# Performance work log

Measured on AMD Instinct MI355X. Metric: run time of the kernel, lower is better.

## Reference

```python
import jax, jax.numpy as jnp
import numpy as np

NUM_NODES = 20000
HIDDEN = 64
NUM_EDGES = 640000
LEAK = 0.2  # PyG GATConv negative_slope default


def gat_conv(x, w, a_src, a_dst, b, src, dst, n):
    # x: [N, F_in]; w: [F_in, H*C]; a_src/a_dst: [H, C]; edges j=src -> i=dst
    H, C = a_src.shape
    xe = (x @ w).reshape(n, H, C)                         # [N, H, C]
    es = jnp.einsum('nhc,hc->nh', xe, a_src)              # alpha_src per node
    ed = jnp.einsum('nhc,hc->nh', xe, a_dst)              # alpha_dst per node
    e = jax.nn.leaky_relu(es[src] + ed[dst], LEAK)        # [E, H] edge logits
    # segment softmax over each destination's incoming edges
    m = jax.ops.segment_max(e, dst, num_segments=n)
    p = jnp.exp(e - m[dst])
    s = jax.ops.segment_sum(p, dst, num_segments=n)
    alpha = p / s[dst]                                    # [E, H]
    out = jax.ops.segment_sum(alpha[:, :, None] * xe[src], dst, num_segments=n)
    return out.reshape(n, H * C) + b                      # concat heads + bias


def setup_inputs() -> dict:
    key = jax.random.key(0)
    ks = jax.random.split(key, 16)
    B, S, N, Hd = 4, 12, NUM_NODES, HIDDEN
    sc = 0.1
    inp = {}
    inp['x'] = jax.random.normal(ks[0], (B, S, N), jnp.float32)
    inp['edge_index'] = jax.random.randint(ks[1], (2, NUM_EDGES), 0, N, jnp.int32)
    inp['proj_w'] = jax.random.normal(ks[2], (S, Hd), jnp.float32) * sc
    inp['proj_b'] = jnp.zeros((Hd,), jnp.float32)
    inp['gat0_w'] = jax.random.normal(ks[3], (Hd, Hd), jnp.float32) * sc
    inp['gat0_asrc'] = jax.random.normal(ks[4], (8, 8), jnp.float32) * sc
    inp['gat0_adst'] = jax.random.normal(ks[5], (8, 8), jnp.float32) * sc
    inp['gat0_b'] = jnp.zeros((Hd,), jnp.float32)
    inp['gat1_w'] = jax.random.normal(ks[6], (Hd, Hd), jnp.float32) * sc
    inp['gat1_asrc'] = jax.random.normal(ks[7], (8, 8), jnp.float32) * sc
    inp['gat1_adst'] = jax.random.normal(ks[8], (8, 8), jnp.float32) * sc
    inp['gat1_b'] = jnp.zeros((Hd,), jnp.float32)
    inp['gat2_w'] = jax.random.normal(ks[9], (Hd, Hd), jnp.float32) * sc
    inp['gat2_asrc'] = jax.random.normal(ks[10], (1, Hd), jnp.float32) * sc
    inp['gat2_adst'] = jax.random.normal(ks[11], (1, Hd), jnp.float32) * sc
    inp['gat2_b'] = jnp.zeros((Hd,), jnp.float32)
    inp['conv_w'] = jax.random.normal(ks[12], (Hd, Hd, 3), jnp.float32) * sc
    inp['conv_b'] = jnp.zeros((Hd,), jnp.float32)
    inp['out_w'] = jax.random.normal(ks[13], (Hd, 3), jnp.float32) * sc
    inp['out_b'] = jnp.zeros((3,), jnp.float32)
    return inp


def reference(x, edge_index, proj_w, proj_b,
              gat0_w, gat0_asrc, gat0_adst, gat0_b,
              gat1_w, gat1_asrc, gat1_adst, gat1_b,
              gat2_w, gat2_asrc, gat2_adst, gat2_b,
              conv_w, conv_b, out_w, out_b):
    B, S, N = x.shape
    # PyG GATConv add_self_loops=True
    loops = jnp.arange(N, dtype=edge_index.dtype)
    src = jnp.concatenate([edge_index[0], loops])
    dst = jnp.concatenate([edge_index[1], loops])
    h = jnp.transpose(x, (0, 2, 1)) @ proj_w + proj_b     # [B, N, Hd]
    layers = [(gat0_w, gat0_asrc, gat0_adst, gat0_b),
              (gat1_w, gat1_asrc, gat1_adst, gat1_b),
              (gat2_w, gat2_asrc, gat2_adst, gat2_b)]
    for i, (w, asr, ads, b) in enumerate(layers):
        h = jax.vmap(lambda hb: gat_conv(hb, w, asr, ads, b, src, dst, N))(h)
        if i < len(layers) - 1:
            h = jax.nn.elu(h)                             # dropout is identity in eval
    hc = jnp.transpose(h, (0, 2, 1))                      # [B, Hd, N]
    hc = jax.lax.conv_general_dilated(hc, conv_w, (1,), ((1, 1),),
                                      dimension_numbers=('NCH', 'OIH', 'NCH'))
    hc = jax.nn.relu(hc + conv_b[None, :, None])
    h = jnp.transpose(hc, (0, 2, 1)) @ out_w + out_b      # [B, N, pred]
    return jnp.transpose(h, (0, 2, 1))                    # [B, pred, N]
```

## Files before the change

### kernel.cpp

```cpp
#include <hip/hip_runtime.h>
#include <math.h>

constexpr int B  = 4;
constexpr int S  = 12;
constexpr int N  = 20000;
constexpr int HD = 64;
constexpr int E0 = 640000;
constexpr int EL = E0 + N;
constexpr int BN = B * N;
constexpr int CAP = 128;

__global__ void scatter_kernel(const int* __restrict__ ei, int* __restrict__ cnt,
                               int* __restrict__ perm) {
    int e = blockIdx.x * blockDim.x + threadIdx.x;
    if (e >= EL) return;
    int s, d;
    if (e < E0) { s = ei[e]; d = ei[E0 + e]; }
    else        { s = e - E0; d = s; }
    int pos = atomicAdd(&cnt[d], 1) & (CAP - 1);
    perm[d * CAP + pos] = s;
}

__global__ void tw_kernel(const float* __restrict__ cw, float* __restrict__ cwD) {
    int i = blockIdx.x * blockDim.x + threadIdx.x;
    if (i >= HD * HD * 3) return;
    int o = i / (HD * 3), rem = i % (HD * 3), c = rem / 3, dt = rem % 3;
    cwD[dt * (HD * HD) + c * HD + o] = cw[i];
}

constexpr int GT = 64;

template<int H>
__global__ __launch_bounds__(256, 4)
void gemm_attn_kernel(const float* __restrict__ hin, const float* __restrict__ w,
                      const float* __restrict__ asrc, const float* __restrict__ adst,
                      float* __restrict__ xe, float* __restrict__ es, float* __restrict__ ed) {
    __shared__ float tile[GT * HD];
    int base = blockIdx.x * GT;
    for (int i = threadIdx.x; i < GT * (HD / 4); i += 256)
        ((float4*)tile)[i] = ((const float4*)(hin + (size_t)base * HD))[i];
    int lane = threadIdx.x & 63;
    float wres[HD];
    #pragma unroll
    for (int c = 0; c < HD; ++c) wres[c] = w[c * HD + lane];
    float as_ = asrc[lane], ad_ = adst[lane];
    __syncthreads();
    int wvid = threadIdx.x >> 6;
    for (int j = wvid * 16; j < wvid * 16 + 16; ++j) {
        int t = base + j;
        float acc = 0.f;
        #pragma unroll
        for (int cq = 0; cq < 16; ++cq) {
            float4 r = ((const float4*)tile)[j * 16 + cq];
            acc = fmaf(r.x, wres[4 * cq + 0], acc);
            acc = fmaf(r.y, wres[4 * cq + 1], acc);
            acc = fmaf(r.z, wres[4 * cq + 2], acc);
            acc = fmaf(r.w, wres[4 * cq + 3], acc);
        }
        xe[(size_t)t * HD + lane] = acc;
        float t0 = acc * as_, t1 = acc * ad_;
        if (H == 8) {
            #pragma unroll
            for (int m = 1; m < 8; m <<= 1) {
                t0 += __shfl_xor(t0, m, 64);
                t1 += __shfl_xor(t1, m, 64);
            }
            if ((lane & 7) == 0) {
                es[t * 8 + (lane >> 3)] = t0;
                ed[t * 8 + (lane >> 3)] = t1;
            }
        } else {
            #pragma unroll
            for (int m = 1; m < 64; m <<= 1) {
                t0 += __shfl_xor(t0, m, 64);
                t1 += __shfl_xor(t1, m, 64);
            }
            if (lane == 0) { es[t] = t0; ed[t] = t1; }
        }
    }
}

__global__ __launch_bounds__(256, 4)
void fused0_kernel(const float* __restrict__ x, const float* __restrict__ pw,
                   const float* __restrict__ pb, const float* __restrict__ w,
                   const float* __restrict__ asrc, const float* __restrict__ adst,
                   float* __restrict__ xe, float* __restrict__ es, float* __restrict__ ed) {
    __shared__ float tile[GT * HD];
    __shared__ float xt[S * GT];
    int base = blockIdx.x * GT;
    for (int i = threadIdx.x; i < S * GT; i += 256) {
        int s = i >> 6, nl = i & 63;
        int t = base + nl, bb = t / N, n = t - bb * N;
        xt[i] = x[(bb * S + s) * N + n];
    }
    int lane = threadIdx.x & 63;
    float wres[HD];
    #pragma unroll
    for (int c = 0; c < HD; ++c) wres[c] = w[c * HD + lane];
    float pwres[S];
    #pragma unroll
    for (int s = 0; s < S; ++s) pwres[s] = pw[s * HD + lane];
    float pbv = pb[lane];
    float as_ = asrc[lane], ad_ = adst[lane];
    __syncthreads();
    int wvid = threadIdx.x >> 6;
    for (int j = wvid * 16; j < wvid * 16 + 16; ++j) {
        float hl = pbv;
        #pragma unroll
        for (int s = 0; s < S; ++s)
            hl = fmaf(xt[s * GT + j], pwres[s], hl);
        tile[j * HD + lane] = hl;
    }
    for (int j = wvid * 16; j < wvid * 16 + 16; ++j) {
        int t = base + j;
        float acc = 0.f;
        #pragma unroll
        for (int cq = 0; cq < 16; ++cq) {
            float4 r = ((const float4*)tile)[j * 16 + cq];
            acc = fmaf(r.x, wres[4 * cq + 0], acc);
            acc = fmaf(r.y, wres[4 * cq + 1], acc);
            acc = fmaf(r.z, wres[4 * cq + 2], acc);
            acc = fmaf(r.w, wres[4 * cq + 3], acc);
        }
        xe[(size_t)t * HD + lane] = acc;
        float t0 = acc * as_, t1 = acc * ad_;
        #pragma unroll
        for (int m = 1; m < 8; m <<= 1) {
            t0 += __shfl_xor(t0, m, 64);
            t1 += __shfl_xor(t1, m, 64);
        }
        if ((lane & 7) == 0) {
            es[t * 8 + (lane >> 3)] = t0;
            ed[t * 8 + (lane >> 3)] = t1;
        }
    }
}

template<int H, bool DO_ELU>
__global__ __launch_bounds__(256, 8)
void agg_kernel(const float* __restrict__ xe, const float* __restrict__ es,
                const float* __restrict__ ed, const int* __restrict__ cnt,
                const int* __restrict__ perm, const float* __restrict__ bias,
                float* __restrict__ hout) {
    int g = blockIdx.x;
    int bb   = (g & 7) >> 1;
    int idx  = (g >> 3) * 2 + (g & 1);
    int node = idx * 4 + (threadIdx.x >> 6);
    int lane  = threadIdx.x & 63;
    int group = lane >> 4;
    int c4    = lane & 15;
    int deg = cnt[node];
    int baseE = node * CAP;
    int h = (H == 8) ? (c4 >> 1) : 0;
    const float*  es_b = es + bb * (N * H);
    const float4* xe4  = (const float4*)(xe + bb * (N * HD));
    float edv = ed[(bb * N + node) * H + h];
    float4 acc = {0.f, 0.f, 0.f, 0.f};
    float ssum = 0.f;
    #pragma unroll 4
    for (int jb = 0; jb < deg; jb += 4) {
        int j = jb + group;
        bool valid = (j < deg);
        int src = perm[baseE + (valid ? j : 0)];
        float e = es_b[src * H + h] + edv;
        e = fmaxf(e, 0.2f * e);
        float p = valid ? __expf(e) : 0.f;
        ssum += p;
        float4 xv = xe4[src * 16 + c4];
        acc.x = fmaf(p, xv.x, acc.x);
        acc.y = fmaf(p, xv.y, acc.y);
        acc.z = fmaf(p, xv.z, acc.z);
        acc.w = fmaf(p, xv.w, acc.w);
    }
    #pragma unroll
    for (int m = 16; m < 64; m <<= 1) {
        acc.x += __shfl_xor(acc.x, m, 64);
        acc.y += __shfl_xor(acc.y, m, 64);
        acc.z += __shfl_xor(acc.z, m, 64);
        acc.w += __shfl_xor(acc.w, m, 64);
        ssum  += __shfl_xor(ssum,  m, 64);
    }
    if (lane < 16) {
        float inv = 1.f / ssum;
        const float4* b4 = (const float4*)bias;
        float4 bv = b4[c4];
        float4 r;
        r.x = acc.x * inv + bv.x;
        r.y = acc.y * inv + bv.y;
        r.z = acc.z * inv + bv.z;
        r.w = acc.w * inv + bv.w;
        if (DO_ELU) {
            r.x = (r.x > 0.f) ? r.x : expm1f(r.x);
            r.y = (r.y > 0.f) ? r.y : expm1f(r.y);
            r.z = (r.z > 0.f) ? r.z : expm1f(r.z);
            r.w = (r.w > 0.f) ? r.w : expm1f(r.w);
        }
        ((float4*)hout)[(bb * N + node) * 16 + c4] = r;
    }
}

constexpr int CVN = 16;
__global__ __launch_bounds__(64, 2)
void conv_out_kernel(const float* __restrict__ h, const float* __restrict__ cwD,
                     const float* __restrict__ cb, const float* __restrict__ ow,
                     const float* __restrict__ ob, float* __restrict__ out) {
    __shared__ float part[CVN * HD];
    int bb = blockIdx.y;
    int base = blockIdx.x * CVN;
    int lane = threadIdx.x;
    float cbv = cb[lane];
    float ow0 = ow[lane * 3 + 0], ow1 = ow[lane * 3 + 1], ow2 = ow[lane * 3 + 2];
    float ob0 = ob[0], ob1 = ob[1], ob2 = ob[2];
    #pragma unroll
    for (int j = 0; j < CVN; ++j) part[j * HD + lane] = cbv;
    #pragma unroll 1
    for (int dt = 0; dt < 3; ++dt) {
        float wres[HD];
        #pragma unroll
        for (int c = 0; c < HD; ++c) wres[c] = cwD[dt * (HD * HD) + c * HD + lane];
        #pragma unroll 2
        for (int j = 0; j < CVN; ++j) {
            int m = base + j + dt - 1;
            if (m >= 0 && m < N) {
                const float* hp = h + ((size_t)bb * N + m) * HD;
                float a = 0.f;
                #pragma unroll
                for (int c = 0; c < HD; ++c)
                    a = fmaf(hp[c], wres[c], a);
                part[j * HD + lane] += a;
            }
        }
    }
    #pragma unroll 1
    for (int j = 0; j < CVN; ++j) {
        float v = fmaxf(part[j * HD + lane], 0.f);
        float t0 = v * ow0, t1 = v * ow1, t2 = v * ow2;
        #pragma unroll
        for (int m = 1; m < 64; m <<= 1) {
            t0 += __shfl_xor(t0, m, 64);
            t1 += __shfl_xor(t1, m, 64);
            t2 += __shfl_xor(t2, m, 64);
        }
        int n = base + j;
        if (lane < 3) {
            float r = (lane == 0) ? t0 + ob0 : (lane == 1) ? t1 + ob1 : t2 + ob2;
            out[(size_t)bb * 3 * N + lane * N + n] = r;
        }
    }
}

extern "C" void kernel_launch(void* const* d_in, const int* in_sizes, int n_in,
                              void* d_out, int out_size, void* d_ws, size_t ws_size,
                              hipStream_t stream) {
    const float* x      = (const float*)d_in[0];
    const int*   ei     = (const int*)  d_in[1];
    const float* proj_w = (const float*)d_in[2];
    const float* proj_b = (const float*)d_in[3];
    const float* g_w [3] = {(const float*)d_in[4], (const float*)d_in[8],  (const float*)d_in[12]};
    const float* g_as[3] = {(const float*)d_in[5], (const float*)d_in[9],  (const float*)d_in[13]};
    const float* g_ad[3] = {(const float*)d_in[6], (const float*)d_in[10], (const float*)d_in[14]};
    const float* g_b [3] = {(const float*)d_in[7], (const float*)d_in[11], (const float*)d_in[15]};
    const float* conv_w = (const float*)d_in[16];
    const float* conv_b = (const float*)d_in[17];
    const float* out_w  = (const float*)d_in[18];
    const float* out_b  = (const float*)d_in[19];
    float* out = (float*)d_out;

    float* bufA = (float*)d_ws;
    float* bufX = bufA + (size_t)BN * HD;
    float* es   = bufX + (size_t)BN * HD;
    float* ed   = es   + (size_t)BN * 8;
    int* cnt  = (int*)(ed + (size_t)BN * 8);
    int* perm = cnt + N;
    float* cwD = (float*)(perm + (size_t)N * CAP);

    const int TB = 256;
    const int gE = (EL + TB - 1) / TB;

    hipMemsetAsync(cnt, 0, N * sizeof(int), stream);
    scatter_kernel<<<gE, TB, 0, stream>>>(ei, cnt, perm);

    tw_kernel<<<(HD * HD * 3 + TB - 1) / TB, TB, 0, stream>>>(conv_w, cwD);

    fused0_kernel<<<BN / GT, TB, 0, stream>>>(x, proj_w, proj_b, g_w[0], g_as[0], g_ad[0],
                                              bufX, es, ed);
    agg_kernel<8, true><<<BN / 4, TB, 0, stream>>>(bufX, es, ed, cnt, perm, g_b[0], bufA);

    gemm_attn_kernel<8><<<BN / GT, TB, 0, stream>>>(bufA, g_w[1], g_as[1], g_ad[1], bufX, es, ed);
    agg_kernel<8, true><<<BN / 4, TB, 0, stream>>>(bufX, es, ed, cnt, perm, g_b[1], bufA);

    gemm_attn_kernel<1><<<BN / GT, TB, 0, stream>>>(bufA, g_w[2], g_as[2], g_ad[2], bufX, es, ed);
    agg_kernel<1, false><<<BN / 4, TB, 0, stream>>>(bufX, es, ed, cnt, perm, g_b[2], bufA);

    conv_out_kernel<<<dim3(N / CVN, B), 64, 0, stream>>>(bufA, cwD, conv_b, out_w, out_b, out);
}
```

Measured before the change: 442.6 us.

## Stage conv input rows in shared memory and split output rows across two waves

The conv+output kernel now loads the 18 input rows (with halo) for a 16-node tile into shared memory with float4 loads, replacing per-lane redundant global reads of each row. Two wavefronts each handle 8 output nodes with register accumulators instead of an LDS partial buffer, and the weight slice is loaded in two 32-channel halves to cut register pressure. This reduces global traffic and raises occupancy in exchange for a block barrier and more weight reloads per block.

```diff
diff --git a/kernel.cpp b/kernel.cpp
--- a/kernel.cpp
+++ b/kernel.cpp
@@ -199,41 +199,59 @@
     }
 }
 
-constexpr int CVN = 16;
-__global__ __launch_bounds__(64, 2)
+constexpr int CV2 = 16;
+__global__ __launch_bounds__(128, 4)
 void conv_out_kernel(const float* __restrict__ h, const float* __restrict__ cwD,
                      const float* __restrict__ cb, const float* __restrict__ ow,
                      const float* __restrict__ ob, float* __restrict__ out) {
-    __shared__ float part[CVN * HD];
+    __shared__ alignas(16) float tile[(CV2 + 2) * HD];
     int bb = blockIdx.y;
-    int base = blockIdx.x * CVN;
-    int lane = threadIdx.x;
+    int base = blockIdx.x * CV2;
+    const float4* hb4 = (const float4*)(h + (size_t)bb * N * HD);
+    for (int i = threadIdx.x; i < (CV2 + 2) * (HD / 4); i += 128) {
+        int r = i >> 4;
+        int m = base + r - 1;
+        float4 v = make_float4(0.f, 0.f, 0.f, 0.f);
+        if (m >= 0 && m < N) v = hb4[(size_t)m * 16 + (i & 15)];
+        ((float4*)tile)[i] = v;
+    }
+    int lane = threadIdx.x & 63;
+    int wvid = threadIdx.x >> 6;
     float cbv = cb[lane];
     float ow0 = ow[lane * 3 + 0], ow1 = ow[lane * 3 + 1], ow2 = ow[lane * 3 + 2];
     float ob0 = ob[0], ob1 = ob[1], ob2 = ob[2];
-    #pragma unroll
-    for (int j = 0; j < CVN; ++j) part[j * HD + lane] = cbv;
+    float acc[8];
+    #pragma unroll
+    for (int j = 0; j < 8; ++j) acc[j] = cbv;
+    __syncthreads();
     #pragma unroll 1
     for (int dt = 0; dt < 3; ++dt) {
-        float wres[HD];
-        #pragma unroll
-        for (int c = 0; c < HD; ++c) wres[c] = cwD[dt * (HD * HD) + c * HD + lane];
-        #pragma unroll 2
-        for (int j = 0; j < CVN; ++j) {
-            int m = base + j + dt - 1;
-            if (m >= 0 && m < N) {
-                const float* hp = h + ((size_t)bb * N + m) * HD;
+        #pragma unroll 1
+        for (int ch = 0; ch < 2; ++ch) {
+            float wres[32];
+            #pragma unroll
+            for (int c = 0; c < 32; ++c)
+                wres[c] = cwD[dt * (HD * HD) + (ch * 32 + c) * HD + lane];
+            #pragma unroll
+            for (int j = 0; j < 8; ++j) {
+                const float4* row =
+                    (const float4*)(tile + (wvid * 8 + j + dt) * HD + ch * 32);
                 float a = 0.f;
                 #pragma unroll
-                for (int c = 0; c < HD; ++c)
-                    a = fmaf(hp[c], wres[c], a);
-                part[j * HD + lane] += a;
+                for (int cq = 0; cq < 8; ++cq) {
+                    float4 r = row[cq];
+                    a = fmaf(r.x, wres[4 * cq + 0], a);
+                    a = fmaf(r.y, wres[4 * cq + 1], a);
+                    a = fmaf(r.z, wres[4 * cq + 2], a);
+                    a = fmaf(r.w, wres[4 * cq + 3], a);
+                }
+                acc[j] += a;
             }
         }
     }
-    #pragma unroll 1
-    for (int j = 0; j < CVN; ++j) {
-        float v = fmaxf(part[j * HD + lane], 0.f);
+    #pragma unroll
+    for (int j = 0; j < 8; ++j) {
+        float v = fmaxf(acc[j], 0.f);
         float t0 = v * ow0, t1 = v * ow1, t2 = v * ow2;
         #pragma unroll
         for (int m = 1; m < 64; m <<= 1) {
@@ -241,7 +259,7 @@
             t1 += __shfl_xor(t1, m, 64);
             t2 += __shfl_xor(t2, m, 64);
         }
-        int n = base + j;
+        int n = base + wvid * 8 + j;
         if (lane < 3) {
             float r = (lane == 0) ? t0 + ob0 : (lane == 1) ? t1 + ob1 : t2 + ob2;
             out[(size_t)bb * 3 * N + lane * N + n] = r;
@@ -292,5 +310,5 @@
     gemm_attn_kernel<1><<<BN / GT, TB, 0, stream>>>(bufA, g_w[2], g_as[2], g_ad[2], bufX, es, ed);
     agg_kernel<1, false><<<BN / 4, TB, 0, stream>>>(bufX, es, ed, cnt, perm, g_b[2], bufA);
 
-    conv_out_kernel<<<dim3(N / CVN, B), 64, 0, stream>>>(bufA, cwD, conv_b, out_w, out_b, out);
-}
+    conv_out_kernel<<<dim3(N / CV2, B), 128, 0, stream>>>(bufA, cwD, conv_b, out_w, out_b, out);
+}
```

Result: slower. 456.3 us (+3.1%).
